# Performance work log

Measured on AMD Instinct MI355X. Metric: run time of the kernel, lower is better.

The kernel has to match this reference:

```python
import jax, jax.numpy as jnp
import numpy as np

B, T, NN, H = 16, 64, 4096, 1024  # batch, seq_len, num_nodes**2, gru hidden


def _gru_layer(x, w_ih, w_hh, b_ih, b_hh):
    """PyTorch-semantics GRU layer, batch_first. x: [B, T, in] -> [B, T, H]."""
    h_dim = w_hh.shape[1]
    # precompute all input-side gate projections in one GEMM: [B, T, 3H]
    gates_x = jnp.einsum('bti,gi->btg', x, w_ih) + b_ih

    def step(h, gx):
        gh = h @ w_hh.T + b_hh                      # [B, 3H]
        xr, xz, xn = jnp.split(gx, 3, axis=-1)
        hr, hz, hn = jnp.split(gh, 3, axis=-1)
        r = jax.nn.sigmoid(xr + hr)
        z = jax.nn.sigmoid(xz + hz)
        n = jnp.tanh(xn + r * hn)
        h_new = (1.0 - z) * n + z * h
        return h_new, h_new

    h0 = jnp.zeros((x.shape[0], h_dim), x.dtype)
    _, ys = jax.lax.scan(step, h0, jnp.swapaxes(gates_x, 0, 1))  # time-major scan
    return jnp.swapaxes(ys, 0, 1)


def setup_inputs() -> dict:
    key = jax.random.key(0)
    ks = jax.random.split(key, 12)
    s_in, s_h = 1.0 / np.sqrt(NN), 1.0 / np.sqrt(H)
    return {
        'x':       jax.random.normal(ks[0], (B, T, NN), jnp.float32),
        'w_ih_l0': jax.random.normal(ks[1], (3 * H, NN), jnp.float32) * s_in,
        'w_hh_l0': jax.random.normal(ks[2], (3 * H, H), jnp.float32) * s_h,
        'b_ih_l0': jax.random.normal(ks[3], (3 * H,), jnp.float32) * s_h,
        'b_hh_l0': jax.random.normal(ks[4], (3 * H,), jnp.float32) * s_h,
        'w_ih_l1': jax.random.normal(ks[5], (3 * H, H), jnp.float32) * s_h,
        'w_hh_l1': jax.random.normal(ks[6], (3 * H, H), jnp.float32) * s_h,
        'b_ih_l1': jax.random.normal(ks[7], (3 * H,), jnp.float32) * s_h,
        'b_hh_l1': jax.random.normal(ks[8], (3 * H,), jnp.float32) * s_h,
        'dec_w':   jax.random.normal(ks[9], (NN, H), jnp.float32) * s_h,
        'dec_b':   jax.random.normal(ks[10], (NN,), jnp.float32) * s_h,
    }


def reference(x, w_ih_l0, w_hh_l0, b_ih_l0, b_hh_l0,
              w_ih_l1, w_hh_l1, b_ih_l1, b_hh_l1, dec_w, dec_b):
    # 2-layer GRU encode (batch_first), no dropout (eval / drop_p=0)
    h1 = _gru_layer(x, w_ih_l0, w_hh_l0, b_ih_l0, b_hh_l0)
    h2 = _gru_layer(h1, w_ih_l1, w_hh_l1, b_ih_l1, b_hh_l1)
    last = h2[:, -1, :]                               # [B, H] last timestep
    # per-sample decoder loop in the original == one batched GEMM here
    pred_graph_adj = last @ dec_w.T + dec_b           # [B, num_nodes**2]
    return pred_graph_adj
```

## Files before the change

### kernel.cpp

```cpp
#include <hip/hip_runtime.h>
#include <math.h>

constexpr int kB = 16;
constexpr int kT = 64;
constexpr int kH = 1024;

typedef short bf16x8 __attribute__((ext_vector_type(8)));
typedef float floatx4 __attribute__((ext_vector_type(4)));

__device__ __forceinline__ unsigned short f2bf_rne(float f) {
    unsigned u = __float_as_uint(f);
    u = u + 0x7FFFu + ((u >> 16) & 1u);
    return (unsigned short)(u >> 16);
}
__device__ __forceinline__ unsigned f2bf_fast_u(float f) {
    return (__float_as_uint(f) + 0x8000u) >> 16;
}

__device__ __forceinline__ void store_short_sys(unsigned short* p, unsigned v) {
    asm volatile("global_store_short %0, %1, off sc0 sc1"
                 :: "v"(p), "v"(v) : "memory");
}
__device__ __forceinline__ void store_dword_sys(unsigned* p, unsigned v) {
    asm volatile("global_store_dword %0, %1, off sc0 sc1"
                 :: "v"(p), "v"(v) : "memory");
}
__device__ __forceinline__ unsigned load_dword_sys(const unsigned* p) {
    unsigned v;
    asm volatile("global_load_dword %0, %1, off sc0 sc1\n\t"
                 "s_waitcnt vmcnt(0)"
                 : "=v"(v) : "v"(p) : "memory");
    return v;
}

__device__ __forceinline__ void gload_lds16(const unsigned short* g,
                                            unsigned short* lds) {
    __builtin_amdgcn_global_load_lds(
        (const __attribute__((address_space(1))) unsigned int*)(g),
        (__attribute__((address_space(3))) unsigned int*)(lds), 16, 0, 0);
}

__global__ __launch_bounds__(256)
void pack_bf16(const float* __restrict__ src, unsigned short* __restrict__ dst,
               int n4)
{
    const int i = blockIdx.x * 256 + threadIdx.x;
    if (i < n4) {
        const float4 v = ((const float4*)src)[i];
        ushort4 o;
        o.x = f2bf_rne(v.x); o.y = f2bf_rne(v.y);
        o.z = f2bf_rne(v.z); o.w = f2bf_rne(v.w);
        ((ushort4*)dst)[i] = o;
    }
}

#define GBM 64
#define GBN 64
#define GBK 16
#define GPAD 4

__global__ __launch_bounds__(256)
void gemm_nt_bias(const float* __restrict__ X, const float* __restrict__ W,
                  const float* __restrict__ bias, float* __restrict__ C,
                  int M, int N, int K)
{
    __shared__ float Xs[GBK][GBM + GPAD];
    __shared__ float Ws[GBK][GBN + GPAD];

    const int tid = threadIdx.x;
    const int bm = blockIdx.y * GBM;
    const int bn = blockIdx.x * GBN;
    const int tm = (tid >> 4) * 4;
    const int tn = (tid & 15) * 4;
    const int lr = tid >> 2;
    const int lc = (tid & 3) * 4;

    float acc[4][4] = {};

    for (int k0 = 0; k0 < K; k0 += GBK) {
        {
            const int gr = bm + lr;
            float4 v = make_float4(0.f, 0.f, 0.f, 0.f);
            if (gr < M) v = *(const float4*)(X + (long)gr * K + k0 + lc);
            Xs[lc + 0][lr] = v.x; Xs[lc + 1][lr] = v.y;
            Xs[lc + 2][lr] = v.z; Xs[lc + 3][lr] = v.w;
        }
        {
            const int gr = bn + lr;
            const float4 v = *(const float4*)(W + (long)gr * K + k0 + lc);
            Ws[lc + 0][lr] = v.x; Ws[lc + 1][lr] = v.y;
            Ws[lc + 2][lr] = v.z; Ws[lc + 3][lr] = v.w;
        }
        __syncthreads();
        #pragma unroll
        for (int k = 0; k < GBK; ++k) {
            const float4 a4 = *(const float4*)&Xs[k][tm];
            const float4 b4 = *(const float4*)&Ws[k][tn];
            acc[0][0] += a4.x * b4.x; acc[0][1] += a4.x * b4.y; acc[0][2] += a4.x * b4.z; acc[0][3] += a4.x * b4.w;
            acc[1][0] += a4.y * b4.x; acc[1][1] += a4.y * b4.y; acc[1][2] += a4.y * b4.z; acc[1][3] += a4.y * b4.w;
            acc[2][0] += a4.z * b4.x; acc[2][1] += a4.z * b4.y; acc[2][2] += a4.z * b4.z; acc[2][3] += a4.z * b4.w;
            acc[3][0] += a4.w * b4.x; acc[3][1] += a4.w * b4.y; acc[3][2] += a4.w * b4.z; acc[3][3] += a4.w * b4.w;
        }
        __syncthreads();
    }

    #pragma unroll
    for (int i = 0; i < 4; ++i) {
        const int gr = bm + tm + i;
        if (gr >= M) continue;
        #pragma unroll
        for (int jj = 0; jj < 4; ++jj) {
            const int gc = bn + tn + jj;
            C[(long)gr * N + gc] = acc[i][jj] + bias[gc];
        }
    }
}

__global__ __launch_bounds__(256)
void gemm_bf16_a(const unsigned short* __restrict__ X,
                 const unsigned short* __restrict__ W,
                 const float* __restrict__ bias,
                 float* __restrict__ C,
                 int M, int N, int K)
{
    __shared__ __attribute__((aligned(16))) unsigned short As[4][64 * 32];
    __shared__ __attribute__((aligned(16))) unsigned short Bs[4][128 * 32];

    const int tid  = threadIdx.x;
    const int lane = tid & 63;
    const int w    = tid >> 6;
    const int wm   = w & 1;
    const int wn   = w >> 1;
    const int al   = lane & 15;
    const int aq   = lane >> 4;

    const int bid = blockIdx.x;
    const int swz = (bid & 7) * 48 + (bid >> 3);
    const int bn  = (swz % 24) * 128;
    const int bm  = (swz / 24) * 64;

    const int srow = lane >> 2;
    const int scol = (lane & 3) * 8;

    const int nT = K / 32;

    #define ISSUE_A(buf, k0c)                                                  \
        gload_lds16(X + (size_t)(bm + w * 16 + srow) * K + (k0c) + scol,       \
                    &As[buf][(w * 16) * 32]);                                  \
        gload_lds16(W + (size_t)(bn + w * 32 + srow) * K + (k0c) + scol,       \
                    &Bs[buf][(w * 32) * 32]);                                  \
        gload_lds16(W + (size_t)(bn + w * 32 + 16 + srow) * K + (k0c) + scol,  \
                    &Bs[buf][(w * 32 + 16) * 32]);

    floatx4 acc[2][4];
    #pragma unroll
    for (int i = 0; i < 2; ++i)
        #pragma unroll
        for (int j = 0; j < 4; ++j)
            acc[i][j] = (floatx4){0.f, 0.f, 0.f, 0.f};

    ISSUE_A(0, 0);
    ISSUE_A(1, 32);

    for (int t = 0; t < nT; ++t) {
        const int k2 = (t + 2 < nT) ? (t + 2) * 32 : t * 32;
        const int b2 = (t + 2) & 3;
        ISSUE_A(b2, k2);

        asm volatile("s_waitcnt vmcnt(6)" ::: "memory");
        __builtin_amdgcn_s_barrier();
        asm volatile("" ::: "memory");

        const int cb = t & 3;
        bf16x8 af[2], bf[4];
        #pragma unroll
        for (int i = 0; i < 2; ++i)
            af[i] = *(const bf16x8*)&As[cb][(wm * 32 + i * 16 + al) * 32 + aq * 8];
        #pragma unroll
        for (int j = 0; j < 4; ++j)
            bf[j] = *(const bf16x8*)&Bs[cb][(wn * 64 + j * 16 + al) * 32 + aq * 8];
        #pragma unroll
        for (int i = 0; i < 2; ++i)
            #pragma unroll
            for (int j = 0; j < 4; ++j)
                acc[i][j] = __builtin_amdgcn_mfma_f32_16x16x32_bf16(
                    af[i], bf[j], acc[i][j], 0, 0, 0);

        asm volatile("" ::: "memory");
        __builtin_amdgcn_s_barrier();
    }
    #undef ISSUE_A

    #pragma unroll
    for (int i = 0; i < 2; ++i) {
        #pragma unroll
        for (int j = 0; j < 4; ++j) {
            const int row0 = bm + wm * 32 + i * 16 + aq * 4;
            const int col  = bn + wn * 64 + j * 16 + al;
            const float bv = bias[col];
            #pragma unroll
            for (int r = 0; r < 4; ++r)
                C[(long)(row0 + r) * N + col] = acc[i][j][r] + bv;
        }
    }
}

#define FLAG_STRIDE 4

__global__ __launch_bounds__(768, 3)
void fused_gru_persistent(const float* __restrict__ gx0,
                          const unsigned short* __restrict__ w0, const float* __restrict__ bb0,
                          const unsigned short* __restrict__ w1, const float* __restrict__ bb1,
                          const unsigned short* __restrict__ w2, const float* __restrict__ bb2,
                          unsigned short* __restrict__ h1bf0, unsigned short* __restrict__ h1bf1,
                          unsigned short* __restrict__ h2bf0, unsigned short* __restrict__ h2bf1,
                          float* __restrict__ h2last, unsigned* __restrict__ flags)
{
    __shared__ __attribute__((aligned(16))) floatx4 part[12][3][64];

    const int tid   = threadIdx.x;
    const int lane  = tid & 63;
    const int wid   = tid >> 6;
    const int bx    = blockIdx.x;
    const int jbase = bx * 16;

    const int m  = wid >> 2;
    const int kh = wid & 3;
    const int al = lane & 15;
    const int aq = lane >> 4;

    const unsigned short* Wm = (m == 0) ? w0 : (m == 1) ? w1 : w2;
    const long wbase = (long)(jbase + al) * kH + kh * 256 + aq * 8;
    bf16x8 wreg[3][8];
    #pragma unroll
    for (int g = 0; g < 3; ++g)
        #pragma unroll
        for (int s = 0; s < 8; ++s)
            wreg[g][s] = *(const bf16x8*)(Wm + (long)g * kH * kH + wbase + s * 32);

    const int ub  = tid >> 4;
    const int ujj = tid & 15;
    const int ujg = jbase + ujj;
    const float b0r = bb0[ujg], b0z = bb0[kH + ujg], b0n = bb0[2 * kH + ujg];
    const float b1r = bb1[ujg], b1z = bb1[kH + ujg], b1n = bb1[2 * kH + ujg];
    const float b2r = bb2[ujg], b2z = bb2[kH + ujg], b2n = bb2[2 * kH + ujg];

    float h1reg = 0.f;
    float h2reg = 0.f;

    const int aoff = al * kH + kh * 256 + aq * 8;
    const int pl   = (ub >> 2) * 16 + ujj;
    const int pr   = ub & 3;

    float gxr = 0.f, gxz = 0.f, gxn = 0.f;
    if (tid < 256) {
        const float* g = gx0 + (long)ub * (kT * 3 * kH);
        gxr = g[ujg]; gxz = g[kH + ujg]; gxn = g[2 * kH + ujg];
    }

    for (int k = 0; k <= kT; ++k) {
        const unsigned short* h1p = (k & 1) ? h1bf0 : h1bf1;
        unsigned short*       h1o = (k & 1) ? h1bf1 : h1bf0;
        const unsigned short* h2p = (k & 1) ? h2bf1 : h2bf0;
        unsigned short*       h2o = (k & 1) ? h2bf0 : h2bf1;

        const bool azero = (m < 2) ? (k == 0) : (k <= 1);
        const unsigned short* hsrc = (m < 2) ? h1p : h2p;
        bf16x8 a[8];
        if (!azero) {
            #pragma unroll
            for (int s = 0; s < 8; ++s)
                asm volatile("global_load_dwordx4 %0, %1, off sc0 sc1"
                             : "=&v"(a[s]) : "v"(hsrc + aoff + s * 32) : "memory");
            asm volatile("s_waitcnt vmcnt(0)" ::: "memory");
            __builtin_amdgcn_sched_barrier(0);
        } else {
            #pragma unroll
            for (int s = 0; s < 8; ++s)
                a[s] = (bf16x8){0, 0, 0, 0, 0, 0, 0, 0};
        }

        floatx4 acc[3];
        #pragma unroll
        for (int g = 0; g < 3; ++g) acc[g] = (floatx4){0.f, 0.f, 0.f, 0.f};
        #pragma unroll
        for (int s = 0; s < 8; ++s)
            #pragma unroll
            for (int g = 0; g < 3; ++g)
                acc[g] = __builtin_amdgcn_mfma_f32_16x16x32_bf16(
                    a[s], wreg[g][s], acc[g], 0, 0, 0);

        #pragma unroll
        for (int g = 0; g < 3; ++g)
            part[wid][g][lane] = acc[g];
        __syncthreads();

        if (tid < 256) {
            float gh[3][3];
            #pragma unroll
            for (int mm = 0; mm < 3; ++mm)
                #pragma unroll
                for (int g = 0; g < 3; ++g)
                    gh[mm][g] = part[mm * 4 + 0][g][pl][pr] + part[mm * 4 + 1][g][pl][pr]
                              + part[mm * 4 + 2][g][pl][pr] + part[mm * 4 + 3][g][pl][pr];

            if (k < kT) {
                const float hr = gh[0][0] + b0r;
                const float hz = gh[0][1] + b0z;
                const float hn = gh[0][2] + b0n;
                const float r = 1.f / (1.f + __expf(-(gxr + hr)));
                const float z = 1.f / (1.f + __expf(-(gxz + hz)));
                const float n = tanhf(gxn + r * hn);
                const float hnew = (1.f - z) * n + z * h1reg;
                h1reg = hnew;
                store_short_sys(h1o + ub * kH + ujg, f2bf_fast_u(hnew));
            }
            if (k > 0) {
                const float xr = gh[1][0] + b1r;
                const float xz = gh[1][1] + b1z;
                const float xn = gh[1][2] + b1n;
                const float hr = gh[2][0] + b2r;
                const float hz = gh[2][1] + b2z;
                const float hn = gh[2][2] + b2n;
                const float r = 1.f / (1.f + __expf(-(xr + hr)));
                const float z = 1.f / (1.f + __expf(-(xz + hz)));
                const float n = tanhf(xn + r * hn);
                const float hnew = (1.f - z) * n + z * h2reg;
                h2reg = hnew;
                store_short_sys(h2o + ub * kH + ujg, f2bf_fast_u(hnew));
                if (k == kT) h2last[(long)ub * kH + ujg] = hnew;
            }
        }

        float nxr = 0.f, nxz = 0.f, nxn = 0.f;
        if (tid < 256 && (k + 1) < kT) {
            const float* g = gx0 + (long)ub * (kT * 3 * kH) + (long)(k + 1) * 3 * kH;
            nxr = g[ujg]; nxz = g[kH + ujg]; nxn = g[2 * kH + ujg];
        }

        if (k < kT) {
            __syncthreads();
            if (wid == 0) {
                const unsigned gen = (unsigned)(k + 1);
                if (lane == 0)
                    store_dword_sys(&flags[bx * FLAG_STRIDE], gen);
                while (load_dword_sys(&flags[lane * FLAG_STRIDE]) < gen) {}
            }
            __syncthreads();
        }

        gxr = nxr; gxz = nxz; gxn = nxn;
    }
}

extern "C" void kernel_launch(void* const* d_in, const int* in_sizes, int n_in,
                              void* d_out, int out_size, void* d_ws, size_t ws_size,
                              hipStream_t stream)
{
    const float* x        = (const float*)d_in[0];
    const float* w_ih_l0  = (const float*)d_in[1];
    const float* w_hh_l0  = (const float*)d_in[2];
    const float* b_ih_l0  = (const float*)d_in[3];
    const float* b_hh_l0  = (const float*)d_in[4];
    const float* w_ih_l1  = (const float*)d_in[5];
    const float* w_hh_l1  = (const float*)d_in[6];
    const float* b_ih_l1  = (const float*)d_in[7];
    const float* b_hh_l1  = (const float*)d_in[8];
    const float* dec_w    = (const float*)d_in[9];
    const float* dec_b    = (const float*)d_in[10];
    float* out = (float*)d_out;

    float* ws    = (float*)d_ws;
    float* gx0   = ws;
    unsigned short* h1bf0 = (unsigned short*)(gx0 + (size_t)1024 * 3072);
    unsigned short* h1bf1 = h1bf0 + (size_t)kB * kH;
    unsigned short* h2bf0 = h1bf1 + (size_t)kB * kH;
    unsigned short* h2bf1 = h2bf0 + (size_t)kB * kH;
    float* h2last = (float*)(h2bf1 + (size_t)kB * kH);
    unsigned short* wbf0 = (unsigned short*)(h2last + (size_t)kB * kH);
    unsigned short* wbf1 = wbf0 + (size_t)3 * kH * kH;
    unsigned short* wbf2 = wbf1 + (size_t)3 * kH * kH;
    unsigned short* xbf  = wbf2 + (size_t)3 * kH * kH;
    unsigned short* wihbf = xbf + (size_t)1024 * 4096;
    unsigned* flags = (unsigned*)(wihbf + (size_t)3072 * 4096);

    (void)hipMemsetAsync(flags, 0, 4096, stream);

    const int wn4 = 3 * kH * kH / 4;
    const int xn4 = 1024 * 4096 / 4;
    const int win4 = 3072 * 4096 / 4;

    pack_bf16<<<(wn4 + 255) / 256, 256, 0, stream>>>(w_hh_l0, wbf0, wn4);
    pack_bf16<<<(wn4 + 255) / 256, 256, 0, stream>>>(w_ih_l1, wbf1, wn4);
    pack_bf16<<<(wn4 + 255) / 256, 256, 0, stream>>>(w_hh_l1, wbf2, wn4);
    pack_bf16<<<(xn4 + 255) / 256, 256, 0, stream>>>(x, xbf, xn4);
    pack_bf16<<<(win4 + 255) / 256, 256, 0, stream>>>(w_ih_l0, wihbf, win4);

    gemm_bf16_a<<<384, 256, 0, stream>>>(
        xbf, wihbf, b_ih_l0, gx0, 1024, 3072, 4096);

    fused_gru_persistent<<<64, 768, 0, stream>>>(
        gx0, wbf0, b_hh_l0, wbf1, b_ih_l1, wbf2, b_hh_l1,
        h1bf0, h1bf1, h2bf0, h2bf1, h2last, flags);

    gemm_nt_bias<<<dim3(4096 / GBN, 1), 256, 0, stream>>>(
        h2last, dec_w, dec_b, out, kB, 4096, 1024);
}
```

Before: 666.4 us.

## Fuse input-projection GEMM into persistent GRU kernel with chunked readiness flags

Merges the layer-0 input-projection GEMM into the persistent GRU kernel. Blocks 64 and up compute the GEMM in time-chunk-ordered tiles and publish per-tile ready flags, while the 64 recurrent blocks spin on those flags before reading the gx values they need. This lets the recurrence start before the whole GEMM finishes, and it also merges the five pack kernels into one launch. The risks are a smaller, less efficient GEMM tile (4 of 12 waves only load data), possible deadlock if the GRU blocks are not co-resident with the GEMM blocks, and extra flag polling on the recurrent critical path.

```diff
diff --git a/kernel.cpp b/kernel.cpp
--- a/kernel.cpp
+++ b/kernel.cpp
@@ -32,6 +32,16 @@
                  : "=v"(v) : "v"(p) : "memory");
     return v;
 }
+__device__ __forceinline__ void load3_float_sys(const float* p0, const float* p1,
+                                                const float* p2,
+                                                float& a, float& b, float& c) {
+    asm volatile("global_load_dword %0, %3, off sc0 sc1\n\t"
+                 "global_load_dword %1, %4, off sc0 sc1\n\t"
+                 "global_load_dword %2, %5, off sc0 sc1\n\t"
+                 "s_waitcnt vmcnt(0)"
+                 : "=&v"(a), "=&v"(b), "=&v"(c)
+                 : "v"(p0), "v"(p1), "v"(p2) : "memory");
+}
 
 __device__ __forceinline__ void gload_lds16(const unsigned short* g,
                                             unsigned short* lds) {
@@ -41,17 +51,28 @@
 }
 
 __global__ __launch_bounds__(256)
-void pack_bf16(const float* __restrict__ src, unsigned short* __restrict__ dst,
-               int n4)
+void pack_bf16_multi(const float* __restrict__ s0, unsigned short* __restrict__ d0, int n0,
+                     const float* __restrict__ s1, unsigned short* __restrict__ d1, int n1,
+                     const float* __restrict__ s2, unsigned short* __restrict__ d2, int n2,
+                     const float* __restrict__ s3, unsigned short* __restrict__ d3, int n3,
+                     const float* __restrict__ s4, unsigned short* __restrict__ d4, int n4)
 {
-    const int i = blockIdx.x * 256 + threadIdx.x;
-    if (i < n4) {
-        const float4 v = ((const float4*)src)[i];
-        ushort4 o;
-        o.x = f2bf_rne(v.x); o.y = f2bf_rne(v.y);
-        o.z = f2bf_rne(v.z); o.w = f2bf_rne(v.w);
-        ((ushort4*)dst)[i] = o;
-    }
+    int i = blockIdx.x * 256 + threadIdx.x;
+    const float* s; unsigned short* d;
+    if (i < n0) { s = s0; d = d0; }
+    else { i -= n0;
+    if (i < n1) { s = s1; d = d1; }
+    else { i -= n1;
+    if (i < n2) { s = s2; d = d2; }
+    else { i -= n2;
+    if (i < n3) { s = s3; d = d3; }
+    else { i -= n3;
+    if (i >= n4) return; s = s4; d = d4; }}}}
+    const float4 v = ((const float4*)s)[i];
+    ushort4 o;
+    o.x = f2bf_rne(v.x); o.y = f2bf_rne(v.y);
+    o.z = f2bf_rne(v.z); o.w = f2bf_rne(v.w);
+    ((ushort4*)d)[i] = o;
 }
 
 #define GBM 64
@@ -116,113 +137,130 @@
     }
 }
 
-__global__ __launch_bounds__(256)
-void gemm_bf16_a(const unsigned short* __restrict__ X,
-                 const unsigned short* __restrict__ W,
-                 const float* __restrict__ bias,
-                 float* __restrict__ C,
-                 int M, int N, int K)
+#define FLAG_STRIDE 4
+
+__global__ __launch_bounds__(768, 3)
+void fused_mega(const unsigned short* __restrict__ xbf,
+                const unsigned short* __restrict__ wihbf,
+                const float* __restrict__ bih0,
+                float* __restrict__ gx0,
+                const unsigned short* __restrict__ w0, const float* __restrict__ bb0,
+                const unsigned short* __restrict__ w1, const float* __restrict__ bb1,
+                const unsigned short* __restrict__ w2, const float* __restrict__ bb2,
+                unsigned short* __restrict__ h1bf0, unsigned short* __restrict__ h1bf1,
+                unsigned short* __restrict__ h2bf0, unsigned short* __restrict__ h2bf1,
+                float* __restrict__ h2last, unsigned* __restrict__ flags)
 {
-    __shared__ __attribute__((aligned(16))) unsigned short As[4][64 * 32];
-    __shared__ __attribute__((aligned(16))) unsigned short Bs[4][128 * 32];
-
-    const int tid  = threadIdx.x;
+    __shared__ __attribute__((aligned(16))) char smem[49152];
+
+    const int tid = threadIdx.x;
+    const int bx  = blockIdx.x;
     const int lane = tid & 63;
-    const int w    = tid >> 6;
-    const int wm   = w & 1;
-    const int wn   = w >> 1;
-    const int al   = lane & 15;
-    const int aq   = lane >> 4;
-
-    const int bid = blockIdx.x;
-    const int swz = (bid & 7) * 48 + (bid >> 3);
-    const int bn  = (swz % 24) * 128;
-    const int bm  = (swz / 24) * 64;
-
-    const int srow = lane >> 2;
-    const int scol = (lane & 3) * 8;
-
-    const int nT = K / 32;
-
-    #define ISSUE_A(buf, k0c)                                                  \
-        gload_lds16(X + (size_t)(bm + w * 16 + srow) * K + (k0c) + scol,       \
-                    &As[buf][(w * 16) * 32]);                                  \
-        gload_lds16(W + (size_t)(bn + w * 32 + srow) * K + (k0c) + scol,       \
-                    &Bs[buf][(w * 32) * 32]);                                  \
-        gload_lds16(W + (size_t)(bn + w * 32 + 16 + srow) * K + (k0c) + scol,  \
-                    &Bs[buf][(w * 32 + 16) * 32]);
-
-    floatx4 acc[2][4];
-    #pragma unroll
-    for (int i = 0; i < 2; ++i)
-        #pragma unroll
-        for (int j = 0; j < 4; ++j)
-            acc[i][j] = (floatx4){0.f, 0.f, 0.f, 0.f};
-
-    ISSUE_A(0, 0);
-    ISSUE_A(1, 32);
-
-    for (int t = 0; t < nT; ++t) {
-        const int k2 = (t + 2 < nT) ? (t + 2) * 32 : t * 32;
-        const int b2 = (t + 2) & 3;
-        ISSUE_A(b2, k2);
-
-        asm volatile("s_waitcnt vmcnt(6)" ::: "memory");
-        __builtin_amdgcn_s_barrier();
-        asm volatile("" ::: "memory");
-
-        const int cb = t & 3;
-        bf16x8 af[2], bf[4];
-        #pragma unroll
-        for (int i = 0; i < 2; ++i)
-            af[i] = *(const bf16x8*)&As[cb][(wm * 32 + i * 16 + al) * 32 + aq * 8];
-        #pragma unroll
-        for (int j = 0; j < 4; ++j)
-            bf[j] = *(const bf16x8*)&Bs[cb][(wn * 64 + j * 16 + al) * 32 + aq * 8];
-        #pragma unroll
-        for (int i = 0; i < 2; ++i)
+    const int wid  = tid >> 6;
+    unsigned* const gxflags = flags + 256;
+
+    if (bx >= 64) {
+        unsigned short (*As)[2048] = (unsigned short(*)[2048])smem;
+        unsigned short (*Bs)[4096] = (unsigned short(*)[4096])(smem + 16384);
+        const int widx = bx - 64;
+        const int srow = lane >> 2;
+        const int scol = (lane & 3) * 8;
+        const int al = lane & 15;
+        const int aq = lane >> 4;
+        const int wm = wid & 1;
+        const int wn = wid >> 1;
+
+        for (int pass = 0; pass < 2; ++pass) {
+            const int T = widx + pass * 192;
+            const int c = T / 24;
+            const int n = T % 24;
+            const int bn = n * 128;
+
+            const unsigned short* gsrc;
+            int ldsoff;
+            bool isA;
+            if (wid < 4) {
+                const int tr = wid * 16 + srow;
+                const long grow = (long)((tr >> 2) * 64 + c * 4 + (tr & 3));
+                gsrc = xbf + grow * 4096 + scol;
+                ldsoff = wid * 512;
+                isA = true;
+            } else {
+                gsrc = wihbf + (long)(bn + (wid - 4) * 16 + srow) * 4096 + scol;
+                ldsoff = (wid - 4) * 512;
+                isA = false;
+            }
+
+            floatx4 acc[2][2];
             #pragma unroll
-            for (int j = 0; j < 4; ++j)
-                acc[i][j] = __builtin_amdgcn_mfma_f32_16x16x32_bf16(
-                    af[i], bf[j], acc[i][j], 0, 0, 0);
-
-        asm volatile("" ::: "memory");
-        __builtin_amdgcn_s_barrier();
+            for (int i = 0; i < 2; ++i)
+                #pragma unroll
+                for (int j = 0; j < 2; ++j)
+                    acc[i][j] = (floatx4){0.f, 0.f, 0.f, 0.f};
+
+            if (isA) { gload_lds16(gsrc + 0,  &As[0][ldsoff]);
+                       gload_lds16(gsrc + 32, &As[1][ldsoff]); }
+            else     { gload_lds16(gsrc + 0,  &Bs[0][ldsoff]);
+                       gload_lds16(gsrc + 32, &Bs[1][ldsoff]); }
+
+            for (int t = 0; t < 128; ++t) {
+                const int k2 = (t + 2 < 128) ? (t + 2) * 32 : t * 32;
+                const int b2 = (t + 2) & 3;
+                if (isA) gload_lds16(gsrc + k2, &As[b2][ldsoff]);
+                else     gload_lds16(gsrc + k2, &Bs[b2][ldsoff]);
+
+                asm volatile("s_waitcnt vmcnt(2)" ::: "memory");
+                __builtin_amdgcn_s_barrier();
+                asm volatile("" ::: "memory");
+
+                if (wid < 8) {
+                    const int cb = t & 3;
+                    bf16x8 af[2], bfr[2];
+                    #pragma unroll
+                    for (int i = 0; i < 2; ++i)
+                        af[i] = *(const bf16x8*)&As[cb][(wm * 32 + i * 16 + al) * 32 + aq * 8];
+                    #pragma unroll
+                    for (int j = 0; j < 2; ++j)
+                        bfr[j] = *(const bf16x8*)&Bs[cb][(wn * 32 + j * 16 + al) * 32 + aq * 8];
+                    #pragma unroll
+                    for (int i = 0; i < 2; ++i)
+                        #pragma unroll
+                        for (int j = 0; j < 2; ++j)
+                            acc[i][j] = __builtin_amdgcn_mfma_f32_16x16x32_bf16(
+                                af[i], bfr[j], acc[i][j], 0, 0, 0);
+                }
+                asm volatile("" ::: "memory");
+                __builtin_amdgcn_s_barrier();
+            }
+
+            if (wid < 8) {
+                #pragma unroll
+                for (int i = 0; i < 2; ++i) {
+                    #pragma unroll
+                    for (int j = 0; j < 2; ++j) {
+                        const int col = bn + wn * 32 + j * 16 + al;
+                        const float bv = bih0[col];
+                        #pragma unroll
+                        for (int r = 0; r < 4; ++r) {
+                            const int tr = wm * 32 + i * 16 + aq * 4 + r;
+                            const long g = (long)((tr >> 2) * 64 + c * 4 + (tr & 3));
+                            store_dword_sys((unsigned*)&gx0[g * 3072 + col],
+                                            __float_as_uint(acc[i][j][r] + bv));
+                        }
+                    }
+                }
+            }
+            asm volatile("s_waitcnt vmcnt(0)" ::: "memory");
+            __builtin_amdgcn_s_barrier();
+            if (tid == 0) store_dword_sys(&gxflags[c * 24 + n], 1u);
+        }
+        return;
     }
-    #undef ISSUE_A
-
-    #pragma unroll
-    for (int i = 0; i < 2; ++i) {
-        #pragma unroll
-        for (int j = 0; j < 4; ++j) {
-            const int row0 = bm + wm * 32 + i * 16 + aq * 4;
-            const int col  = bn + wn * 64 + j * 16 + al;
-            const float bv = bias[col];
-            #pragma unroll
-            for (int r = 0; r < 4; ++r)
-                C[(long)(row0 + r) * N + col] = acc[i][j][r] + bv;
-        }
-    }
-}
-
-#define FLAG_STRIDE 4
-
-__global__ __launch_bounds__(768, 3)
-void fused_gru_persistent(const float* __restrict__ gx0,
-                          const unsigned short* __restrict__ w0, const float* __restrict__ bb0,
-                          const unsigned short* __restrict__ w1, const float* __restrict__ bb1,
-                          const unsigned short* __restrict__ w2, const float* __restrict__ bb2,
-                          unsigned short* __restrict__ h1bf0, unsigned short* __restrict__ h1bf1,
-                          unsigned short* __restrict__ h2bf0, unsigned short* __restrict__ h2bf1,
-                          float* __restrict__ h2last, unsigned* __restrict__ flags)
-{
-    __shared__ __attribute__((aligned(16))) floatx4 part[12][3][64];
-
-    const int tid   = threadIdx.x;
-    const int lane  = tid & 63;
-    const int wid   = tid >> 6;
-    const int bx    = blockIdx.x;
+
+    floatx4 (*part)[3][64] = (floatx4(*)[3][64])smem;
+
     const int jbase = bx * 16;
+    const int ntile = bx >> 3;
 
     const int m  = wid >> 2;
     const int kh = wid & 3;
@@ -253,9 +291,12 @@
     const int pr   = ub & 3;
 
     float gxr = 0.f, gxz = 0.f, gxn = 0.f;
+    int readyChunk = -1;
     if (tid < 256) {
+        while (load_dword_sys(&gxflags[0 * 24 + ntile]) == 0) {}
+        readyChunk = 0;
         const float* g = gx0 + (long)ub * (kT * 3 * kH);
-        gxr = g[ujg]; gxz = g[kH + ujg]; gxn = g[2 * kH + ujg];
+        load3_float_sys(g + ujg, g + kH + ujg, g + 2 * kH + ujg, gxr, gxz, gxn);
     }
 
     for (int k = 0; k <= kT; ++k) {
@@ -334,8 +375,13 @@
 
         float nxr = 0.f, nxz = 0.f, nxn = 0.f;
         if (tid < 256 && (k + 1) < kT) {
+            const int c2 = (k + 1) >> 2;
+            if (c2 != readyChunk) {
+                while (load_dword_sys(&gxflags[c2 * 24 + ntile]) == 0) {}
+                readyChunk = c2;
+            }
             const float* g = gx0 + (long)ub * (kT * 3 * kH) + (long)(k + 1) * 3 * kH;
-            nxr = g[ujg]; nxz = g[kH + ujg]; nxn = g[2 * kH + ujg];
+            load3_float_sys(g + ujg, g + kH + ujg, g + 2 * kH + ujg, nxr, nxz, nxn);
         }
 
         if (k < kT) {
@@ -389,18 +435,15 @@
     const int wn4 = 3 * kH * kH / 4;
     const int xn4 = 1024 * 4096 / 4;
     const int win4 = 3072 * 4096 / 4;
-
-    pack_bf16<<<(wn4 + 255) / 256, 256, 0, stream>>>(w_hh_l0, wbf0, wn4);
-    pack_bf16<<<(wn4 + 255) / 256, 256, 0, stream>>>(w_ih_l1, wbf1, wn4);
-    pack_bf16<<<(wn4 + 255) / 256, 256, 0, stream>>>(w_hh_l1, wbf2, wn4);
-    pack_bf16<<<(xn4 + 255) / 256, 256, 0, stream>>>(x, xbf, xn4);
-    pack_bf16<<<(win4 + 255) / 256, 256, 0, stream>>>(w_ih_l0, wihbf, win4);
-
-    gemm_bf16_a<<<384, 256, 0, stream>>>(
-        xbf, wihbf, b_ih_l0, gx0, 1024, 3072, 4096);
-
-    fused_gru_persistent<<<64, 768, 0, stream>>>(
-        gx0, wbf0, b_hh_l0, wbf1, b_ih_l1, wbf2, b_hh_l1,
+    const int total4 = wn4 * 3 + xn4 + win4;
+
+    pack_bf16_multi<<<(total4 + 255) / 256, 256, 0, stream>>>(
+        w_hh_l0, wbf0, wn4,  w_ih_l1, wbf1, wn4,  w_hh_l1, wbf2, wn4,
+        x, xbf, xn4,  w_ih_l0, wihbf, win4);
+
+    fused_mega<<<256, 768, 0, stream>>>(
+        xbf, wihbf, b_ih_l0, gx0,
+        wbf0, b_hh_l0, wbf1, b_ih_l1, wbf2, b_hh_l1,
         h1bf0, h1bf1, h2bf0, h2bf1, h2last, flags);
 
     gemm_nt_bias<<<dim3(4096 / GBN, 1), 256, 0, stream>>>(
```

New measurement: 629.4 us. 1.06x faster.
